# Kernel optimization log

Measured on AMD Instinct MI355X. Metric: run time of the kernel, lower is better.

## Reference

```python
import jax, jax.numpy as jnp
import numpy as np

NUM_EXPERTS = 8
TOP_K = 2
D_IN = 1024
D_OUT = 1024
N_TOKENS = 8192


def setup_inputs() -> dict:
    key = jax.random.key(0)
    ks = jax.random.split(key, 7)
    s_in = 1.0 / np.sqrt(D_IN)
    s_out = 1.0 / np.sqrt(D_OUT)
    return {
        "x": jax.random.normal(ks[0], (N_TOKENS, D_IN), dtype=jnp.float32),
        # stacked expert params: fc1 [E, D_in, D_out], fc2 [E, D_out, D_out]
        "W1": jax.random.uniform(ks[1], (NUM_EXPERTS, D_IN, D_OUT), jnp.float32, -s_in, s_in),
        "b1": jax.random.uniform(ks[2], (NUM_EXPERTS, D_OUT), jnp.float32, -s_in, s_in),
        "W2": jax.random.uniform(ks[3], (NUM_EXPERTS, D_OUT, D_OUT), jnp.float32, -s_out, s_out),
        "b2": jax.random.uniform(ks[4], (NUM_EXPERTS, D_OUT), jnp.float32, -s_out, s_out),
        "Wg": jax.random.uniform(ks[5], (D_IN, NUM_EXPERTS), jnp.float32, -s_in, s_in),
        "bg": jax.random.uniform(ks[6], (NUM_EXPERTS,), jnp.float32, -s_in, s_in),
    }


def reference(x, W1, b1, W2, b2, Wg, bg):
    n = x.shape[0]
    # gating
    gate_logits = x @ Wg + bg                      # [N, E]
    gate_weights = jax.nn.softmax(gate_logits, axis=1)
    if TOP_K < NUM_EXPERTS:
        topk_vals, topk_idx = jax.lax.top_k(gate_weights, TOP_K)  # [N, K]
        rows = jnp.arange(n)[:, None]
        gate_weights = jnp.zeros_like(gate_weights).at[rows, topk_idx].set(topk_vals)
    # dense all-expert MLP fan-out (faithful to the original wasteful compute)
    h = jax.nn.relu(jnp.einsum('nd,edh->enh', x, W1) + b1[:, None, :])  # [E, N, H]
    y = jnp.einsum('enh,eho->eno', h, W2) + b2[:, None, :]               # [E, N, O]
    # weighted combine over experts
    out = jnp.einsum('ne,eno->no', gate_weights, y)                      # [N, O]
    return out
```

## Files before the change

### kernel.cpp

```cpp
#include <hip/hip_runtime.h>

#define NUM_E 8
#define N_TOK 8192
#define DIM 1024

typedef __attribute__((ext_vector_type(8))) short short8;
typedef __attribute__((ext_vector_type(4))) float f32x4;

__device__ __forceinline__ unsigned short f2bf(float f) {
  unsigned int u = __float_as_uint(f);
  u = (u + 0x7fffu + ((u >> 16) & 1u)) >> 16;
  return (unsigned short)u;
}

__device__ __forceinline__ void async16(const unsigned short* g, unsigned short* l) {
  __builtin_amdgcn_global_load_lds((const __attribute__((address_space(1))) void*)g,
                                   (__attribute__((address_space(3))) void*)l,
                                   16, 0, 0);
}

__global__ __launch_bounds__(256) void prep_kernel(
    const float* __restrict__ W1, const float* __restrict__ W2,
    unsigned short* __restrict__ W1T, unsigned short* __restrict__ W2T,
    const float* __restrict__ x, const float* __restrict__ Wg,
    const float* __restrict__ bg, int* __restrict__ tok_top,
    float2* __restrict__ tok_wts, unsigned short* __restrict__ xb) {
  __shared__ float s[64][65];
  if (blockIdx.x < 4096) {
    const int bx  = blockIdx.x;
    const int mat = bx >> 8;
    const int tk  = (bx >> 4) & 15;
    const int tn  = bx & 15;
    const float* src;
    unsigned short* dst;
    if (mat < 8) { src = W1 + (size_t)mat * (DIM * DIM); dst = W1T + (size_t)mat * (DIM * DIM); }
    else         { src = W2 + (size_t)(mat - 8) * (DIM * DIM); dst = W2T + (size_t)(mat - 8) * (DIM * DIM); }
    const int k0 = tk * 64, n0 = tn * 64;
    const int t = threadIdx.x;
    {
      const int rr = t >> 4;
      const int c4 = (t & 15) * 4;
#pragma unroll
      for (int i = 0; i < 4; ++i) {
        const int k = i * 16 + rr;
        float4 v = *(const float4*)&src[(size_t)(k0 + k) * DIM + n0 + c4];
        s[c4 + 0][k] = v.x; s[c4 + 1][k] = v.y;
        s[c4 + 2][k] = v.z; s[c4 + 3][k] = v.w;
      }
    }
    __syncthreads();
    {
      const int kq = (t & 7) * 8;
      const int nn = t >> 3;
#pragma unroll
      for (int r = 0; r < 2; ++r) {
        const int n = r * 32 + nn;
        union { unsigned short us[8]; uint4 v; } o;
#pragma unroll
        for (int j = 0; j < 8; ++j) o.us[j] = f2bf(s[n][kq + j]);
        *(uint4*)(dst + (size_t)(n0 + n) * DIM + k0 + kq) = o.v;
      }
    }
  } else {
    const int wave = threadIdx.x >> 6;
    const int lane = threadIdx.x & 63;
    const int n = (blockIdx.x - 4096) * 4 + wave;
    const float4* xr = (const float4*)(x + (size_t)n * DIM);
    unsigned short* xbr = xb + (size_t)n * DIM;
    float acc[NUM_E];
#pragma unroll
    for (int e = 0; e < NUM_E; ++e) acc[e] = 0.f;
#pragma unroll
    for (int it = 0; it < 4; ++it) {
      float4 xv = xr[it * 64 + lane];
      const float4* wr = (const float4*)Wg + (size_t)(it * 256 + lane * 4) * 2;
      float xs[4] = {xv.x, xv.y, xv.z, xv.w};
      union { unsigned short u[4]; uint2 v; } oo;
      oo.u[0] = f2bf(xv.x); oo.u[1] = f2bf(xv.y);
      oo.u[2] = f2bf(xv.z); oo.u[3] = f2bf(xv.w);
      *(uint2*)(xbr + it * 256 + lane * 4) = oo.v;
#pragma unroll
      for (int dd = 0; dd < 4; ++dd) {
        float4 wa = wr[dd * 2 + 0];
        float4 wb = wr[dd * 2 + 1];
        acc[0] += xs[dd] * wa.x; acc[1] += xs[dd] * wa.y;
        acc[2] += xs[dd] * wa.z; acc[3] += xs[dd] * wa.w;
        acc[4] += xs[dd] * wb.x; acc[5] += xs[dd] * wb.y;
        acc[6] += xs[dd] * wb.z; acc[7] += xs[dd] * wb.w;
      }
    }
#pragma unroll
    for (int e = 0; e < NUM_E; ++e)
#pragma unroll
      for (int off = 32; off > 0; off >>= 1)
        acc[e] += __shfl_down(acc[e], off);
    if (lane == 0) {
      float p[NUM_E];
      float mx = -1e30f;
#pragma unroll
      for (int e = 0; e < NUM_E; ++e) { p[e] = acc[e] + bg[e]; mx = fmaxf(mx, p[e]); }
      float ss = 0.f;
#pragma unroll
      for (int e = 0; e < NUM_E; ++e) { p[e] = expf(p[e] - mx); ss += p[e]; }
      float inv = 1.f / ss;
      int i0 = 0;
#pragma unroll
      for (int e = 1; e < NUM_E; ++e) if (p[e] > p[i0]) i0 = e;
      int i1 = (i0 == 0) ? 1 : 0;
#pragma unroll
      for (int e = 0; e < NUM_E; ++e) if (e != i0 && p[e] > p[i1]) i1 = e;
      tok_top[n] = i0 | (i1 << 8);
      tok_wts[n] = make_float2(p[i0] * inv, p[i1] * inv);
    }
  }
}

__global__ __launch_bounds__(1024) void gate2_kernel(const int* __restrict__ tok_top,
                                                     const float2* __restrict__ tok_wts,
                                                     int* __restrict__ counts,
                                                     int* __restrict__ tok_idx,
                                                     float* __restrict__ tok_w) {
  const int e = blockIdx.x;
  const int t = threadIdx.x;
  const int lane = t & 63;
  const int wave = t >> 6;
  __shared__ int wsum[16];
  __shared__ int blocktot;
  int match[8];
  float w[8];
  int cnt = 0;
#pragma unroll
  for (int j = 0; j < 8; ++j) {
    int n = t * 8 + j;
    int top = tok_top[n];
    float2 ww = tok_wts[n];
    bool m0 = (top & 0xff) == e;
    bool m1 = ((top >> 8) & 0xff) == e;
    match[j] = (m0 || m1) ? 1 : 0;
    w[j] = m0 ? ww.x : ww.y;
    cnt += match[j];
  }
  int inc = cnt;
#pragma unroll
  for (int off = 1; off < 64; off <<= 1) {
    int v = __shfl_up(inc, off);
    if (lane >= off) inc += v;
  }
  if (lane == 63) wsum[wave] = inc;
  __syncthreads();
  if (t < 16) {
    int v = wsum[t];
    int s = v;
#pragma unroll
    for (int off = 1; off < 16; off <<= 1) {
      int u = __shfl_up(s, off);
      if (lane >= off) s += u;
    }
    wsum[t] = s - v;
    if (t == 15) blocktot = s;
  }
  __syncthreads();
  int slot = wsum[wave] + inc - cnt;
#pragma unroll
  for (int j = 0; j < 8; ++j) {
    if (match[j]) {
      tok_idx[e * N_TOK + slot] = t * 8 + j;
      tok_w[e * N_TOK + slot] = w[j];
      slot++;
    }
  }
  if (t == 0) counts[e] = blocktot;
}


__device__ __forceinline__ void stage32(const unsigned short* A_src, size_t aOff0, size_t aOff1,
                                        const unsigned short* wte, size_t bOff0, size_t bOff1,
                                        int kk, int kl, int c0, int c1,
                                        unsigned short* sa, unsigned short* sb) {
  async16(A_src + aOff0 + kk + kl, sa + c0);
  async16(A_src + aOff1 + kk + kl, sa + c1);
  async16(wte + bOff0 + kk + kl, sb + c0);
  async16(wte + bOff1 + kk + kl, sb + c1);
}

__device__ __forceinline__ void compute32(const unsigned short* sa, const unsigned short* sb,
                                          int wm, int wn, int lane, f32x4 (&acc)[4][4]) {
  short8 af[4], bfr[4];
#pragma unroll
  for (int i = 0; i < 4; ++i)
    af[i] = *(const short8*)&sa[(wm * 4 + i) * 512 + lane * 8];
#pragma unroll
  for (int j = 0; j < 4; ++j)
    bfr[j] = *(const short8*)&sb[(wn * 4 + j) * 512 + lane * 8];
#pragma unroll
  for (int i = 0; i < 4; ++i)
#pragma unroll
    for (int j = 0; j < 4; ++j)
      acc[i][j] = __builtin_amdgcn_mfma_f32_16x16x32_bf16(af[i], bfr[j], acc[i][j], 0, 0, 0);
}

template <bool FC1>
__global__ __launch_bounds__(256, 4) void moe_gemm_kernel(
    const unsigned short* __restrict__ A_src,
    const unsigned short* __restrict__ wT,
    const float* __restrict__ bias,
    const int* __restrict__ counts,
    const int* __restrict__ tok_idx,
    const float* __restrict__ tok_w,
    unsigned short* __restrict__ h_out,
    float* __restrict__ out)
{
  const int y = blockIdx.y;
  int e = -1, m0 = 0, base = 0;
  {
    int acc_tiles = 0, acc_rows = 0;
#pragma unroll
    for (int i = 0; i < NUM_E; ++i) {
      int c = counts[i];
      int t = (c + 127) >> 7;
      if (y >= acc_tiles && y < acc_tiles + t) {
        e = i; m0 = (y - acc_tiles) * 128; base = acc_rows;
      }
      acc_tiles += t;
      acc_rows += t * 128;
    }
  }
  if (e < 0) return;
  const int count = counts[e];
  const int n0 = blockIdx.x * 128;

  const int tid  = threadIdx.x;
  const int wave = tid >> 6;
  const int lane = tid & 63;
  const int l15  = lane & 15;
  const int quad = lane >> 4;
  const int wm   = wave & 1;
  const int wn   = wave >> 1;

  __shared__ unsigned short sA[2 * 4096];
  __shared__ unsigned short sB[2 * 4096];
  __shared__ int   s_tok[128];
  __shared__ float s_w[128];

  if (!FC1 && tid < 128) {
    int slot = m0 + tid;
    int cs = slot < count ? slot : count - 1;
    s_tok[tid] = tok_idx[e * N_TOK + cs];
    s_w[tid]   = slot < count ? tok_w[e * N_TOK + slot] : 0.f;
  }

  const int r0 = 32 * wave + l15;
  const int r1 = r0 + 16;
  size_t aOff0, aOff1;
  if (FC1) {
    int s0 = m0 + r0; s0 = s0 < count ? s0 : count - 1;
    int s1 = m0 + r1; s1 = s1 < count ? s1 : count - 1;
    aOff0 = (size_t)tok_idx[e * N_TOK + s0] * DIM;
    aOff1 = (size_t)tok_idx[e * N_TOK + s1] * DIM;
  } else {
    aOff0 = (size_t)(base + m0 + r0) * DIM;
    aOff1 = (size_t)(base + m0 + r1) * DIM;
  }
  const unsigned short* wte = wT + (size_t)e * DIM * DIM;
  const size_t bOff0 = (size_t)(n0 + r0) * DIM;
  const size_t bOff1 = (size_t)(n0 + r1) * DIM;
  const int kl = quad * 8;
  const int c0 = (2 * wave + 0) * 512;
  const int c1 = (2 * wave + 1) * 512;

  const f32x4 vzero = {0.f, 0.f, 0.f, 0.f};
  f32x4 acc[4][4];
#pragma unroll
  for (int i = 0; i < 4; ++i)
#pragma unroll
    for (int j = 0; j < 4; ++j) acc[i][j] = vzero;

  stage32(A_src, aOff0, aOff1, wte, bOff0, bOff1, 0, kl, c0, c1, &sA[0], &sB[0]);
  __syncthreads();
  for (int kt = 0; kt < 32; kt += 2) {
    stage32(A_src, aOff0, aOff1, wte, bOff0, bOff1, (kt + 1) * 32, kl, c0, c1,
            &sA[4096], &sB[4096]);
    compute32(&sA[0], &sB[0], wm, wn, lane, acc);
    __syncthreads();
    if (kt + 2 < 32)
      stage32(A_src, aOff0, aOff1, wte, bOff0, bOff1, (kt + 2) * 32, kl, c0, c1,
              &sA[0], &sB[0]);
    compute32(&sA[4096], &sB[4096], wm, wn, lane, acc);
    __syncthreads();
  }

  float bv[4];
#pragma unroll
  for (int j = 0; j < 4; ++j)
    bv[j] = bias[e * DIM + n0 + (wn * 4 + j) * 16 + l15];

  if (FC1) {
#pragma unroll
    for (int i = 0; i < 4; ++i) {
      const int rbase = (wm * 4 + i) * 16 + quad * 4;
#pragma unroll
      for (int r = 0; r < 4; ++r) {
        const int slot = m0 + rbase + r;
        if (slot < count) {
          unsigned short* hp = h_out + (size_t)(base + slot) * DIM + n0;
#pragma unroll
          for (int j = 0; j < 4; ++j) {
            float v = acc[i][j][r] + bv[j];
            v = v > 0.f ? v : 0.f;
            hp[(wn * 4 + j) * 16 + l15] = f2bf(v);
          }
        }
      }
    }
  } else {
#pragma unroll
    for (int i = 0; i < 4; ++i) {
      const int rbase = (wm * 4 + i) * 16 + quad * 4;
#pragma unroll
      for (int r = 0; r < 4; ++r) {
        const int slot = m0 + rbase + r;
        if (slot < count) {
          const int rl = rbase + r;
          const int tok = s_tok[rl];
          const float w = s_w[rl];
          float* op = out + (size_t)tok * DIM + n0;
#pragma unroll
          for (int j = 0; j < 4; ++j) {
            float v = acc[i][j][r] + bv[j];
            atomicAdd(&op[(wn * 4 + j) * 16 + l15], w * v);
          }
        }
      }
    }
  }
}


extern "C" void kernel_launch(void* const* d_in, const int* in_sizes, int n_in,
                              void* d_out, int out_size, void* d_ws, size_t ws_size,
                              hipStream_t stream) {
  const float* x  = (const float*)d_in[0];
  const float* W1 = (const float*)d_in[1];
  const float* b1 = (const float*)d_in[2];
  const float* W2 = (const float*)d_in[3];
  const float* b2 = (const float*)d_in[4];
  const float* Wg = (const float*)d_in[5];
  const float* bg = (const float*)d_in[6];
  float* out = (float*)d_out;

  char* ws = (char*)d_ws;
  int*            counts  = (int*)(ws);
  int*            tok_idx = (int*)(ws + 1024);
  float*          tok_w   = (float*)(ws + 263168);
  unsigned short* xb      = (unsigned short*)(ws + 525312);
  unsigned short* w1t     = (unsigned short*)(ws + 525312 + 16777216ull);
  unsigned short* w2t     = (unsigned short*)(ws + 525312 + 2ull * 16777216ull);
  unsigned short* hb      = (unsigned short*)(ws + 525312 + 3ull * 16777216ull);
  size_t gate_off = 525312 + 3ull * 16777216ull + 35651584ull;
  int*            tok_top = (int*)(ws + gate_off);
  float2*         tok_wts = (float2*)(ws + gate_off + 32768);

  hipMemsetAsync(d_out, 0, (size_t)N_TOK * DIM * sizeof(float), stream);

  prep_kernel<<<4096 + 2048, 256, 0, stream>>>(W1, W2, w1t, w2t,
                                               x, Wg, bg, tok_top, tok_wts, xb);
  gate2_kernel<<<NUM_E, 1024, 0, stream>>>(tok_top, tok_wts, counts, tok_idx, tok_w);
  moe_gemm_kernel<true><<<dim3(8, 136), 256, 0, stream>>>(
      xb, w1t, b1, counts, tok_idx, tok_w, hb, nullptr);
  moe_gemm_kernel<false><<<dim3(8, 136), 256, 0, stream>>>(
      hb, w2t, b2, counts, tok_idx, tok_w, nullptr, out);
}
```

Before: 382.6 us.

## Enlarge MoE GEMM tiles to 256x256 with 8 waves and interleaved MFMA scheduling

Replaces the 128x128 tile, 4-wave GEMM with a 256x256 tile handled by 8 waves, using a 64-wide K step and 128KB of double-buffered LDS. The loop splits each step into quadrant MFMA phases, staging the next tile's A and B between them, with explicit barriers, waitcnts, sched_barrier and setprio. The aim is to raise arithmetic intensity and overlap global loads with MFMA work. In exchange it runs one block per CU, fewer blocks overall (4x72), and pads each expert's rows to 256, which adds padding waste and leaves CUs idle at the tail.

```diff
diff --git a/kernel.cpp b/kernel.cpp
--- a/kernel.cpp
+++ b/kernel.cpp
@@ -173,34 +173,52 @@
 }
 
 
-__device__ __forceinline__ void stage32(const unsigned short* A_src, size_t aOff0, size_t aOff1,
-                                        const unsigned short* wte, size_t bOff0, size_t bOff1,
-                                        int kk, int kl, int c0, int c1,
-                                        unsigned short* sa, unsigned short* sb) {
-  async16(A_src + aOff0 + kk + kl, sa + c0);
-  async16(A_src + aOff1 + kk + kl, sa + c1);
-  async16(wte + bOff0 + kk + kl, sb + c0);
-  async16(wte + bOff1 + kk + kl, sb + c1);
-}
-
-__device__ __forceinline__ void compute32(const unsigned short* sa, const unsigned short* sb,
-                                          int wm, int wn, int lane, f32x4 (&acc)[4][4]) {
-  short8 af[4], bfr[4];
-#pragma unroll
-  for (int i = 0; i < 4; ++i)
-    af[i] = *(const short8*)&sa[(wm * 4 + i) * 512 + lane * 8];
-#pragma unroll
-  for (int j = 0; j < 4; ++j)
-    bfr[j] = *(const short8*)&sb[(wn * 4 + j) * 512 + lane * 8];
-#pragma unroll
-  for (int i = 0; i < 4; ++i)
-#pragma unroll
-    for (int j = 0; j < 4; ++j)
-      acc[i][j] = __builtin_amdgcn_mfma_f32_16x16x32_bf16(af[i], bfr[j], acc[i][j], 0, 0, 0);
-}
+#define BAR()    __builtin_amdgcn_s_barrier()
+#define SCHED0() __builtin_amdgcn_sched_barrier(0)
+#define LGKM0()  { asm volatile("s_waitcnt lgkmcnt(0)" ::: "memory"); SCHED0(); }
+#define VMC0()   { asm volatile("s_waitcnt vmcnt(0)" ::: "memory"); SCHED0(); }
+
+#define STAGE_A(BUFB, KT) { \
+  async16(A_src + aOff0 + (KT) * 64,      sAB + (BUFB) + stg0); \
+  async16(A_src + aOff1 + (KT) * 64,      sAB + (BUFB) + stg1); \
+  async16(A_src + aOff0 + (KT) * 64 + 32, sAB + (BUFB) + 8192 + stg0); \
+  async16(A_src + aOff1 + (KT) * 64 + 32, sAB + (BUFB) + 8192 + stg1); }
+
+#define STAGE_B(BUFB, KT) { \
+  async16(wTe + bOff0 + (KT) * 64,      sAB + 32768 + (BUFB) + stg0); \
+  async16(wTe + bOff1 + (KT) * 64,      sAB + 32768 + (BUFB) + stg1); \
+  async16(wTe + bOff0 + (KT) * 64 + 32, sAB + 32768 + (BUFB) + 8192 + stg0); \
+  async16(wTe + bOff1 + (KT) * 64 + 32, sAB + 32768 + (BUFB) + 8192 + stg1); }
+
+#define DSRA(BUFB, MH) { \
+  _Pragma("unroll") \
+  for (int mi = 0; mi < 4; ++mi) { \
+    a[mi][0] = *(const short8*)(sAB + (BUFB) + rdA + ((MH) * 4 + mi) * 512); \
+    a[mi][1] = *(const short8*)(sAB + (BUFB) + 8192 + rdA + ((MH) * 4 + mi) * 512); \
+  } }
+
+#define DSRB(BUFB, NH, DST) { \
+  _Pragma("unroll") \
+  for (int ni = 0; ni < 2; ++ni) { \
+    DST[ni][0] = *(const short8*)(sAB + (BUFB) + rdB + ((NH) * 2 + ni) * 512); \
+    DST[ni][1] = *(const short8*)(sAB + (BUFB) + 8192 + rdB + ((NH) * 2 + ni) * 512); \
+  } }
+
+#define QMFMA(MH, NH, BSET) { \
+  __builtin_amdgcn_s_setprio(1); \
+  _Pragma("unroll") \
+  for (int mi = 0; mi < 4; ++mi) \
+  _Pragma("unroll") \
+  for (int ni = 0; ni < 2; ++ni) { \
+    acc[(MH) * 4 + mi][(NH) * 2 + ni] = __builtin_amdgcn_mfma_f32_16x16x32_bf16( \
+        a[mi][0], BSET[ni][0], acc[(MH) * 4 + mi][(NH) * 2 + ni], 0, 0, 0); \
+    acc[(MH) * 4 + mi][(NH) * 2 + ni] = __builtin_amdgcn_mfma_f32_16x16x32_bf16( \
+        a[mi][1], BSET[ni][1], acc[(MH) * 4 + mi][(NH) * 2 + ni], 0, 0, 0); \
+  } \
+  __builtin_amdgcn_s_setprio(0); }
 
 template <bool FC1>
-__global__ __launch_bounds__(256, 4) void moe_gemm_kernel(
+__global__ __launch_bounds__(512, 1) void moe_gemm_kernel(
     const unsigned short* __restrict__ A_src,
     const unsigned short* __restrict__ wT,
     const float* __restrict__ bias,
@@ -210,124 +228,116 @@
     unsigned short* __restrict__ h_out,
     float* __restrict__ out)
 {
+  __shared__ unsigned short sAB[65536];
+
   const int y = blockIdx.y;
   int e = -1, m0 = 0, base = 0;
   {
-    int acc_tiles = 0, acc_rows = 0;
+    int at = 0, ar = 0;
 #pragma unroll
     for (int i = 0; i < NUM_E; ++i) {
       int c = counts[i];
-      int t = (c + 127) >> 7;
-      if (y >= acc_tiles && y < acc_tiles + t) {
-        e = i; m0 = (y - acc_tiles) * 128; base = acc_rows;
-      }
-      acc_tiles += t;
-      acc_rows += t * 128;
+      int t = (c + 255) >> 8;
+      if (y >= at && y < at + t) { e = i; m0 = (y - at) * 256; base = ar; }
+      at += t; ar += t * 256;
     }
   }
   if (e < 0) return;
   const int count = counts[e];
-  const int n0 = blockIdx.x * 128;
+  const int n0 = blockIdx.x * 256;
 
   const int tid  = threadIdx.x;
-  const int wave = tid >> 6;
+  const int w    = tid >> 6;
   const int lane = tid & 63;
   const int l15  = lane & 15;
   const int quad = lane >> 4;
-  const int wm   = wave & 1;
-  const int wn   = wave >> 1;
-
-  __shared__ unsigned short sA[2 * 4096];
-  __shared__ unsigned short sB[2 * 4096];
-  __shared__ int   s_tok[128];
-  __shared__ float s_w[128];
-
-  if (!FC1 && tid < 128) {
-    int slot = m0 + tid;
-    int cs = slot < count ? slot : count - 1;
-    s_tok[tid] = tok_idx[e * N_TOK + cs];
-    s_w[tid]   = slot < count ? tok_w[e * N_TOK + slot] : 0.f;
-  }
-
-  const int r0 = 32 * wave + l15;
-  const int r1 = r0 + 16;
-  size_t aOff0, aOff1;
+  const int wr   = w >> 2;
+  const int wc   = w & 3;
+
+  unsigned aOff0, aOff1;
   if (FC1) {
-    int s0 = m0 + r0; s0 = s0 < count ? s0 : count - 1;
-    int s1 = m0 + r1; s1 = s1 < count ? s1 : count - 1;
-    aOff0 = (size_t)tok_idx[e * N_TOK + s0] * DIM;
-    aOff1 = (size_t)tok_idx[e * N_TOK + s1] * DIM;
+    int s0 = m0 + 32 * w + l15;      s0 = s0 < count ? s0 : count - 1;
+    int s1 = m0 + 32 * w + 16 + l15; s1 = s1 < count ? s1 : count - 1;
+    aOff0 = (unsigned)tok_idx[e * N_TOK + s0] * DIM + quad * 8;
+    aOff1 = (unsigned)tok_idx[e * N_TOK + s1] * DIM + quad * 8;
   } else {
-    aOff0 = (size_t)(base + m0 + r0) * DIM;
-    aOff1 = (size_t)(base + m0 + r1) * DIM;
-  }
-  const unsigned short* wte = wT + (size_t)e * DIM * DIM;
-  const size_t bOff0 = (size_t)(n0 + r0) * DIM;
-  const size_t bOff1 = (size_t)(n0 + r1) * DIM;
-  const int kl = quad * 8;
-  const int c0 = (2 * wave + 0) * 512;
-  const int c1 = (2 * wave + 1) * 512;
-
+    aOff0 = (unsigned)(base + m0 + 32 * w + l15) * DIM + quad * 8;
+    aOff1 = aOff0 + 16 * DIM;
+  }
+  const unsigned short* wTe = wT + (size_t)e * DIM * DIM;
+  const unsigned bOff0 = (unsigned)(n0 + 32 * w + l15) * DIM + quad * 8;
+  const unsigned bOff1 = bOff0 + 16 * DIM;
+  const int stg0 = (2 * w + 0) * 512;
+  const int stg1 = (2 * w + 1) * 512;
+  const int rdA = (wr * 8) * 512 + lane * 8;
+  const int rdB = 32768 + (wc * 4) * 512 + lane * 8;
+
+  short8 a[4][2], b01[2][2], b23[2][2];
+  f32x4 acc[8][4];
   const f32x4 vzero = {0.f, 0.f, 0.f, 0.f};
-  f32x4 acc[4][4];
-#pragma unroll
-  for (int i = 0; i < 4; ++i)
+#pragma unroll
+  for (int i = 0; i < 8; ++i)
 #pragma unroll
     for (int j = 0; j < 4; ++j) acc[i][j] = vzero;
 
-  stage32(A_src, aOff0, aOff1, wte, bOff0, bOff1, 0, kl, c0, c1, &sA[0], &sB[0]);
-  __syncthreads();
-  for (int kt = 0; kt < 32; kt += 2) {
-    stage32(A_src, aOff0, aOff1, wte, bOff0, bOff1, (kt + 1) * 32, kl, c0, c1,
-            &sA[4096], &sB[4096]);
-    compute32(&sA[0], &sB[0], wm, wn, lane, acc);
-    __syncthreads();
-    if (kt + 2 < 32)
-      stage32(A_src, aOff0, aOff1, wte, bOff0, bOff1, (kt + 2) * 32, kl, c0, c1,
-              &sA[0], &sB[0]);
-    compute32(&sA[4096], &sB[4096], wm, wn, lane, acc);
-    __syncthreads();
+  STAGE_A(0, 0); STAGE_B(0, 0);
+  VMC0(); BAR();
+
+#pragma unroll 1
+  for (int t = 0; t < 16; ++t) {
+    const int pb = (t & 1) * 16384;
+    const int qb = pb ^ 16384;
+    const int tp = (t + 1 < 16) ? t + 1 : 15;
+    DSRA(pb, 0); DSRB(pb, 0, b01);
+    STAGE_A(qb, tp);
+    BAR(); LGKM0(); QMFMA(0, 0, b01); BAR();
+    DSRB(pb, 1, b23);
+    STAGE_B(qb, tp);
+    BAR(); LGKM0(); QMFMA(0, 1, b23); BAR();
+    DSRA(pb, 1);
+    BAR(); LGKM0(); QMFMA(1, 1, b23); BAR();
+    BAR(); QMFMA(1, 0, b01);
+    VMC0(); BAR();
   }
 
   float bv[4];
 #pragma unroll
   for (int j = 0; j < 4; ++j)
-    bv[j] = bias[e * DIM + n0 + (wn * 4 + j) * 16 + l15];
+    bv[j] = bias[e * DIM + n0 + wc * 64 + j * 16 + l15];
 
   if (FC1) {
 #pragma unroll
-    for (int i = 0; i < 4; ++i) {
-      const int rbase = (wm * 4 + i) * 16 + quad * 4;
+    for (int mi = 0; mi < 8; ++mi) {
+      const int rbase = wr * 128 + mi * 16 + quad * 4;
 #pragma unroll
       for (int r = 0; r < 4; ++r) {
         const int slot = m0 + rbase + r;
         if (slot < count) {
-          unsigned short* hp = h_out + (size_t)(base + slot) * DIM + n0;
+          unsigned short* hp = h_out + (size_t)(base + slot) * DIM + n0 + wc * 64;
 #pragma unroll
           for (int j = 0; j < 4; ++j) {
-            float v = acc[i][j][r] + bv[j];
+            float v = acc[mi][j][r] + bv[j];
             v = v > 0.f ? v : 0.f;
-            hp[(wn * 4 + j) * 16 + l15] = f2bf(v);
+            hp[j * 16 + l15] = f2bf(v);
           }
         }
       }
     }
   } else {
 #pragma unroll
-    for (int i = 0; i < 4; ++i) {
-      const int rbase = (wm * 4 + i) * 16 + quad * 4;
+    for (int mi = 0; mi < 8; ++mi) {
+      const int rbase = wr * 128 + mi * 16 + quad * 4;
 #pragma unroll
       for (int r = 0; r < 4; ++r) {
         const int slot = m0 + rbase + r;
         if (slot < count) {
-          const int rl = rbase + r;
-          const int tok = s_tok[rl];
-          const float w = s_w[rl];
-          float* op = out + (size_t)tok * DIM + n0;
+          const int tok = tok_idx[e * N_TOK + slot];
+          const float wgt = tok_w[e * N_TOK + slot];
+          float* op = out + (size_t)tok * DIM + n0 + wc * 64;
 #pragma unroll
           for (int j = 0; j < 4; ++j) {
-            float v = acc[i][j][r] + bv[j];
-            atomicAdd(&op[(wn * 4 + j) * 16 + l15], w * v);
+            float v = acc[mi][j][r] + bv[j];
+            atomicAdd(&op[j * 16 + l15], wgt * v);
           }
         }
       }
@@ -356,7 +366,7 @@
   unsigned short* w1t     = (unsigned short*)(ws + 525312 + 16777216ull);
   unsigned short* w2t     = (unsigned short*)(ws + 525312 + 2ull * 16777216ull);
   unsigned short* hb      = (unsigned short*)(ws + 525312 + 3ull * 16777216ull);
-  size_t gate_off = 525312 + 3ull * 16777216ull + 35651584ull;
+  size_t gate_off = 525312 + 3ull * 16777216ull + 37748736ull;
   int*            tok_top = (int*)(ws + gate_off);
   float2*         tok_wts = (float2*)(ws + gate_off + 32768);
 
@@ -365,8 +375,8 @@
   prep_kernel<<<4096 + 2048, 256, 0, stream>>>(W1, W2, w1t, w2t,
                                                x, Wg, bg, tok_top, tok_wts, xb);
   gate2_kernel<<<NUM_E, 1024, 0, stream>>>(tok_top, tok_wts, counts, tok_idx, tok_w);
-  moe_gemm_kernel<true><<<dim3(8, 136), 256, 0, stream>>>(
+  moe_gemm_kernel<true><<<dim3(4, 72), 512, 0, stream>>>(
       xb, w1t, b1, counts, tok_idx, tok_w, hb, nullptr);
-  moe_gemm_kernel<false><<<dim3(8, 136), 256, 0, stream>>>(
+  moe_gemm_kernel<false><<<dim3(4, 72), 512, 0, stream>>>(
       hb, w2t, b2, counts, tok_idx, tok_w, nullptr, out);
 }
```

New measurement: 396.3 us. +3.6%, slower.
